# Kernel tuning notes

Hardware: AMD Instinct MI355X
Metric: run time of the kernel (lower is better)

The kernel has to match this reference:

```python
import jax, jax.numpy as jnp
import numpy as np
import math

B, S, D, H = 2, 2048, 1024, 16
DK = D // H


def setup_inputs() -> dict:
    key = jax.random.key(0)
    ks = jax.random.split(key, 12)
    scale = 1.0 / math.sqrt(D)
    inp = {
        "query": jax.random.normal(ks[0], (B, S, D), dtype=jnp.float32),
        "key": jax.random.normal(ks[1], (B, S, D), dtype=jnp.float32),
        "value": jax.random.normal(ks[2], (B, S, D), dtype=jnp.float32),
        # causal mask, broadcastable to [B, H, S, S]; 0 -> masked
        "mask": jnp.tril(jnp.ones((S, S), dtype=jnp.int32))[None, None],
        # linear params stored as [in, out] so y = x @ W + b
        "Wq": jax.random.normal(ks[3], (D, D), dtype=jnp.float32) * scale,
        "bq": jnp.zeros((D,), dtype=jnp.float32),
        "Wk": jax.random.normal(ks[4], (D, D), dtype=jnp.float32) * scale,
        "bk": jnp.zeros((D,), dtype=jnp.float32),
        "Wv": jax.random.normal(ks[5], (D, D), dtype=jnp.float32) * scale,
        "bv": jnp.zeros((D,), dtype=jnp.float32),
        "Wo": jax.random.normal(ks[6], (D, D), dtype=jnp.float32) * scale,
        "bo": jnp.zeros((D,), dtype=jnp.float32),
    }
    return inp


def reference(query, key, value, mask, Wq, bq, Wk, bk, Wv, bv, Wo, bo):
    b = query.shape[0]
    # QKV projections -> [b, H, S, DK]
    q = (query @ Wq + bq).reshape(b, -1, H, DK).transpose(0, 2, 1, 3)
    k = (key @ Wk + bk).reshape(b, -1, H, DK).transpose(0, 2, 1, 3)
    v = (value @ Wv + bv).reshape(b, -1, H, DK).transpose(0, 2, 1, 3)
    # scores [b, H, Sq, Sk]
    scores = jnp.einsum("bhqd,bhkd->bhqk", q, k) / math.sqrt(DK)
    scores = jnp.where(mask == 0, jnp.float32(-1e9), scores)
    attention_weights = jax.nn.softmax(scores, axis=-1)
    # dropout p=0.0 -> identity
    context = jnp.einsum("bhqk,bhkd->bhqd", attention_weights, v)
    context = context.transpose(0, 2, 1, 3).reshape(b, -1, H * DK)
    output = context @ Wo + bo
    return (output, attention_weights)
```

## Files before the change

### kernel.cpp

```cpp
#include <hip/hip_runtime.h>

typedef __bf16 bf16x8 __attribute__((ext_vector_type(8)));
typedef unsigned short u16x8 __attribute__((ext_vector_type(8)));
typedef unsigned short u16x4 __attribute__((ext_vector_type(4)));
typedef unsigned int u32x4 __attribute__((ext_vector_type(4)));
typedef float f32x4 __attribute__((ext_vector_type(4)));

#define MFMA16 __builtin_amdgcn_mfma_f32_16x16x32_bf16

static __device__ inline unsigned short f2bf(float f) {
    unsigned int u = __float_as_uint(f);
    u += 0x7fffu + ((u >> 16) & 1u);
    return (unsigned short)(u >> 16);
}
static __device__ inline unsigned int pack2(float a, float b) {
    return (unsigned int)f2bf(a) | ((unsigned int)f2bf(b) << 16);
}
static __device__ inline bf16x8 as_bf(u16x8 v) { return __builtin_bit_cast(bf16x8, v); }

static __device__ inline void gload_lds16(const unsigned short* g, unsigned short* l) {
    __builtin_amdgcn_global_load_lds(
        (const __attribute__((address_space(1))) void*)g,
        (__attribute__((address_space(3))) void*)l, 16, 0, 0);
}

__global__ __launch_bounds__(256) void conv3(
    const float* __restrict__ A0, const float* __restrict__ A1, const float* __restrict__ A2,
    unsigned short* __restrict__ O0, unsigned short* __restrict__ O1, unsigned short* __restrict__ O2)
{
    const float* A; unsigned short* O;
    switch (blockIdx.y) { case 0: A = A0; O = O0; break;
                          case 1: A = A1; O = O1; break;
                          default: A = A2; O = O2; break; }
    size_t i = ((size_t)blockIdx.x * 256 + threadIdx.x) * 8;
    float4 a = *(const float4*)(A + i);
    float4 b = *(const float4*)(A + i + 4);
    u16x8 o;
    o[0] = f2bf(a.x); o[1] = f2bf(a.y); o[2] = f2bf(a.z); o[3] = f2bf(a.w);
    o[4] = f2bf(b.x); o[5] = f2bf(b.y); o[6] = f2bf(b.z); o[7] = f2bf(b.w);
    *(u16x8*)(O + i) = o;
}

__global__ __launch_bounds__(256) void conv_wt(
    const float* __restrict__ W0, const float* __restrict__ W1,
    const float* __restrict__ W2, const float* __restrict__ W3,
    unsigned short* __restrict__ T0, unsigned short* __restrict__ T1,
    unsigned short* __restrict__ T2, unsigned short* __restrict__ T3)
{
    const float* W; unsigned short* T;
    switch (blockIdx.z) { case 0: W = W0; T = T0; break;
                          case 1: W = W1; T = T1; break;
                          case 2: W = W2; T = T2; break;
                          default: W = W3; T = T3; break; }
    __shared__ unsigned short L[64][72];
    int t = threadIdx.x;
    int r = t >> 2, cs = (t & 3) * 16;
    int r0 = blockIdx.y * 64, c0 = blockIdx.x * 64;
    const float* wp = W + (size_t)(r0 + r) * 1024 + c0 + cs;
    #pragma unroll
    for (int u = 0; u < 16; u += 4) {
        float4 f = *(const float4*)(wp + u);
        L[r][cs + u]     = f2bf(f.x);
        L[r][cs + u + 1] = f2bf(f.y);
        L[r][cs + u + 2] = f2bf(f.z);
        L[r][cs + u + 3] = f2bf(f.w);
    }
    __syncthreads();
    unsigned short* op = T + (size_t)(c0 + r) * 1024 + r0 + cs;
    u16x8 o0, o1;
    #pragma unroll
    for (int i2 = 0; i2 < 8; i2++) { o0[i2] = L[cs + i2][r]; o1[i2] = L[cs + 8 + i2][r]; }
    *(u16x8*)op = o0;
    *(u16x8*)(op + 8) = o1;
}

__global__ __launch_bounds__(256) void proj128(
    const unsigned short* __restrict__ Xq, const unsigned short* __restrict__ Xk,
    const unsigned short* __restrict__ Xv,
    const unsigned short* __restrict__ WqT, const unsigned short* __restrict__ WkT,
    const unsigned short* __restrict__ WvT,
    const float* __restrict__ bq, const float* __restrict__ bk, const float* __restrict__ bv,
    unsigned short* __restrict__ Qo, unsigned short* __restrict__ Ko,
    unsigned short* __restrict__ Vto)
{
    const unsigned short *X, *WT; const float* bias; float oscale;
    if (blockIdx.z == 0)      { X = Xq; WT = WqT; bias = bq; oscale = 0.125f; }
    else if (blockIdx.z == 1) { X = Xk; WT = WkT; bias = bk; oscale = 1.f; }
    else                      { X = Xv; WT = WvT; bias = bv; oscale = 1.f; }
    __shared__ __align__(16) unsigned short Al[128 * 32];
    __shared__ __align__(16) unsigned short Bl[128 * 32];
    const int tid = threadIdx.x, lane = tid & 63, wave = tid >> 6;
    const int li = lane & 15, lg = lane >> 4;
    const int wm = wave >> 1, wn = wave & 1;
    const int row0 = blockIdx.x * 128, n0 = blockIdx.y * 128;
    f32x4 acc[4][4] = {};
    const int srow = wave * 16 + (lane >> 2), sseg = lane & 3;
    const unsigned short* ga0 = X + (size_t)(row0 + srow) * 1024 + sseg * 8;
    const unsigned short* gb0 = WT + (size_t)(n0 + srow) * 1024 + sseg * 8;
    unsigned short* lA = &Al[wave * 512];
    unsigned short* lB = &Bl[wave * 512];
    for (int k0 = 0; k0 < 1024; k0 += 32) {
        gload_lds16(ga0 + k0, lA);
        gload_lds16(ga0 + 64 * 1024 + k0, lA + 2048);
        gload_lds16(gb0 + k0, lB);
        gload_lds16(gb0 + 64 * 1024 + k0, lB + 2048);
        __syncthreads();
        bf16x8 af[4], bfr[4];
        #pragma unroll
        for (int i = 0; i < 4; i++)
            af[i] = as_bf(*(const u16x8*)&Al[(wm * 64 + i * 16 + li) * 32 + lg * 8]);
        #pragma unroll
        for (int j = 0; j < 4; j++)
            bfr[j] = as_bf(*(const u16x8*)&Bl[(wn * 64 + j * 16 + li) * 32 + lg * 8]);
        #pragma unroll
        for (int i = 0; i < 4; i++)
            #pragma unroll
            for (int j = 0; j < 4; j++)
                acc[i][j] = MFMA16(af[i], bfr[j], acc[i][j], 0, 0, 0);
        __syncthreads();
    }
    const int b = row0 >> 11;
    if (blockIdx.z == 2) {
        #pragma unroll
        for (int j = 0; j < 4; j++) {
            int n = n0 + wn * 64 + j * 16 + li;
            float bb = bias[n];
            int h = n >> 6, dk = n & 63;
            unsigned short* ob = Vto + ((size_t)(b * 16 + h) * 64 + dk) * 2048;
            #pragma unroll
            for (int i = 0; i < 4; i++) {
                int s = (row0 + wm * 64 + i * 16 + lg * 4) & 2047;
                u16x4 pk;
                pk[0] = f2bf(acc[i][j][0] + bb);
                pk[1] = f2bf(acc[i][j][1] + bb);
                pk[2] = f2bf(acc[i][j][2] + bb);
                pk[3] = f2bf(acc[i][j][3] + bb);
                *(u16x4*)(ob + s) = pk;
            }
        }
    } else {
        unsigned short* out = (blockIdx.z == 0) ? Qo : Ko;
        #pragma unroll
        for (int j = 0; j < 4; j++) {
            int n = n0 + wn * 64 + j * 16 + li;
            float bb = bias[n];
            int h = n >> 6, dk = n & 63;
            unsigned short* ob = out + ((size_t)(b * 16 + h) * 2048) * 64 + dk;
            #pragma unroll
            for (int i = 0; i < 4; i++)
                #pragma unroll
                for (int r = 0; r < 4; r++) {
                    int s = (row0 + wm * 64 + i * 16 + lg * 4 + r) & 2047;
                    ob[(size_t)s * 64] = f2bf((acc[i][j][r] + bb) * oscale);
                }
        }
    }
}

__global__ __launch_bounds__(256) void final128(
    const unsigned short* __restrict__ A, const unsigned short* __restrict__ WT,
    const float* __restrict__ bias, float* __restrict__ out)
{
    __shared__ __align__(16) unsigned short Al[128 * 32];
    __shared__ __align__(16) unsigned short Bl[128 * 32];
    const int tid = threadIdx.x, lane = tid & 63, wave = tid >> 6;
    const int li = lane & 15, lg = lane >> 4;
    const int wm = wave >> 1, wn = wave & 1;
    const int row0 = blockIdx.x * 128, n0 = blockIdx.y * 128;
    f32x4 acc[4][4] = {};
    const int srow = wave * 16 + (lane >> 2), sseg = lane & 3;
    const unsigned short* ga0 = A + (size_t)(row0 + srow) * 1024 + sseg * 8;
    const unsigned short* gb0 = WT + (size_t)(n0 + srow) * 1024 + sseg * 8;
    unsigned short* lA = &Al[wave * 512];
    unsigned short* lB = &Bl[wave * 512];
    for (int k0 = 0; k0 < 1024; k0 += 32) {
        gload_lds16(ga0 + k0, lA);
        gload_lds16(ga0 + 64 * 1024 + k0, lA + 2048);
        gload_lds16(gb0 + k0, lB);
        gload_lds16(gb0 + 64 * 1024 + k0, lB + 2048);
        __syncthreads();
        bf16x8 af[4], bfr[4];
        #pragma unroll
        for (int i = 0; i < 4; i++)
            af[i] = as_bf(*(const u16x8*)&Al[(wm * 64 + i * 16 + li) * 32 + lg * 8]);
        #pragma unroll
        for (int j = 0; j < 4; j++)
            bfr[j] = as_bf(*(const u16x8*)&Bl[(wn * 64 + j * 16 + li) * 32 + lg * 8]);
        #pragma unroll
        for (int i = 0; i < 4; i++)
            #pragma unroll
            for (int j = 0; j < 4; j++)
                acc[i][j] = MFMA16(af[i], bfr[j], acc[i][j], 0, 0, 0);
        __syncthreads();
    }
    #pragma unroll
    for (int j = 0; j < 4; j++) {
        int n = n0 + wn * 64 + j * 16 + li;
        float bb = bias[n];
        #pragma unroll
        for (int i = 0; i < 4; i++)
            #pragma unroll
            for (int r = 0; r < 4; r++) {
                int row = row0 + wm * 64 + i * 16 + lg * 4 + r;
                out[(size_t)row * 1024 + n] = acc[i][j][r] + bb;
            }
    }
}

__global__ __launch_bounds__(256, 4) void attn_fused(
    const unsigned short* __restrict__ Q, const unsigned short* __restrict__ K,
    const unsigned short* __restrict__ Vt,
    float* __restrict__ wOut, unsigned short* __restrict__ ctx)
{
    __shared__ __align__(16) unsigned short Kl[2][4096];
    __shared__ __align__(16) unsigned short Vl[2][4096];
    const int tid = threadIdx.x, lane = tid & 63, wave = tid >> 6;
    const int li = lane & 15, lg = lane >> 4;
    const int y = blockIdx.y;
    const int bh = blockIdx.x * 4 + (y >> 4);
    const int t = y & 15;
    const int b = bh >> 4, h = bh & 15;
    const unsigned short* Kb = K + (size_t)bh * 2048 * 64;
    const unsigned short* Vb = Vt + (size_t)bh * 64 * 2048;
    const int aSel = 32 * (lg & 1);
    const bool hiT = lg >= 2;

    auto stageK = [&](int u, int buf) {
        const unsigned short* base = Kb + (size_t)u * 64 * 64;
        #pragma unroll
        for (int c = 0; c < 2; c++) {
            int s16 = c * 256 + wave * 64 + lane;
            int row = s16 >> 3, uu = s16 & 7;
            int ul = uu ^ (row & 7);
            gload_lds16(base + row * 64 + ul * 8,
                        &Kl[buf][(size_t)(c * 256 + wave * 64) * 8]);
        }
    };
    auto stageV = [&](int u, int buf) {
        #pragma unroll
        for (int c = 0; c < 2; c++) {
            int s16 = c * 256 + wave * 64 + lane;
            int row = s16 >> 3, uu = s16 & 7;
            int ul = uu ^ (row & 7);
            gload_lds16(Vb + (size_t)row * 2048 + u * 64 + ul * 8,
                        &Vl[buf][(size_t)(c * 256 + wave * 64) * 8]);
        }
    };
    auto kfrag = [&](const unsigned short* KB, int tt, int hf) -> bf16x8 {
        int row = tt * 16 + li;
        int st = ((hf * 4 + lg) ^ (li & 7));
        return as_bf(*(const u16x8*)&KB[row * 64 + st * 8]);
    };
    auto vfrag = [&](const unsigned short* VB, int g, int c2l) -> bf16x8 {
        int row = g * 16 + li;
        int st = ((c2l * 4 + lg) ^ (li & 7));
        return as_bf(*(const u16x8*)&VB[row * 64 + st * 8]);
    };

    #pragma unroll 1
    for (int pass = 0; pass < 2; ++pass) {
        const int Mt = pass ? (31 - t) : t;
        const int q0 = Mt * 64;
        const int M16 = Mt * 4 + wave;
        const int nun = Mt + 1;
        const unsigned short* Qp = Q + ((size_t)bh * 2048 + q0 + wave * 16 + li) * 64 + lg * 8;
        bf16x8 qa0 = as_bf(*(const u16x8*)Qp);
        bf16x8 qa1 = as_bf(*(const u16x8*)(Qp + 32));

        float lsum = 0.f;
        stageK(0, 0);
        __syncthreads();
        #pragma unroll 1
        for (int u = 0; u < nun; ++u) {
            if (u + 1 < nun) stageK(u + 1, (u + 1) & 1);
            const unsigned short* KB = &Kl[u & 1][0];
            #pragma unroll
            for (int tt = 0; tt < 4; tt++) {
                int kts = u * 4 + tt;
                if (kts <= M16) {
                    f32x4 s = {0.f, 0.f, 0.f, 0.f};
                    s = MFMA16(kfrag(KB, tt, 0), qa0, s, 0, 0, 0);
                    s = MFMA16(kfrag(KB, tt, 1), qa1, s, 0, 0, 0);
                    if (kts < M16) {
                        lsum += __expf(s[0]) + __expf(s[1]) + __expf(s[2]) + __expf(s[3]);
                    } else {
                        #pragma unroll
                        for (int r = 0; r < 4; r++)
                            if (lg * 4 + r <= li) lsum += __expf(s[r]);
                    }
                }
            }
            __syncthreads();
        }
        lsum += __shfl_xor(lsum, 16);
        lsum += __shfl_xor(lsum, 32);
        const float rinv = 1.f / lsum;

        stageK(0, 0);
        stageV(0, 0);
        __syncthreads();
        float* wRow = wOut + (size_t)bh * 2048 * 2048 + (size_t)(q0 + wave * 16 + li) * 2048;
        f32x4 o0 = {}, o1 = {}, o2 = {}, o3 = {};
        #pragma unroll 1
        for (int u = 0; u < nun; ++u) {
            if (u + 1 < nun) { stageK(u + 1, (u + 1) & 1); stageV(u + 1, (u + 1) & 1); }
            const unsigned short* KB = &Kl[u & 1][0];
            const unsigned short* VB = &Vl[u & 1][0];
            #pragma unroll
            for (int c2l = 0; c2l < 2; c2l++) {
                unsigned pk0, pk1, pk2, pk3;
                #pragma unroll
                for (int st = 0; st < 2; st++) {
                    int kts = u * 4 + c2l * 2 + st;
                    f32x4 w = {0.f, 0.f, 0.f, 0.f};
                    if (kts <= M16) {
                        f32x4 s = {0.f, 0.f, 0.f, 0.f};
                        int tt = c2l * 2 + st;
                        s = MFMA16(kfrag(KB, tt, 0), qa0, s, 0, 0, 0);
                        s = MFMA16(kfrag(KB, tt, 1), qa1, s, 0, 0, 0);
                        bool diag = (kts == M16);
                        #pragma unroll
                        for (int r = 0; r < 4; r++) {
                            float pv = __expf(s[r]);
                            if (diag && (lg * 4 + r) > li) pv = 0.f;
                            w[r] = pv * rinv;
                        }
                    }
                    *(f32x4*)(wRow + kts * 16 + lg * 4) = w;
                    if (st == 0) { pk0 = pack2(w[0], w[1]); pk1 = pack2(w[2], w[3]); }
                    else         { pk2 = pack2(w[0], w[1]); pk3 = pack2(w[2], w[3]); }
                }
                if (u * 4 + c2l * 2 <= M16) {
                    int srcA = li + aSel, srcB = srcA + 16;
                    unsigned ga0v = __shfl(pk0, srcA), ga1v = __shfl(pk1, srcA);
                    unsigned ga2v = __shfl(pk2, srcA), ga3v = __shfl(pk3, srcA);
                    unsigned gb0v = __shfl(pk0, srcB), gb1v = __shfl(pk1, srcB);
                    unsigned gb2v = __shfl(pk2, srcB), gb3v = __shfl(pk3, srcB);
                    u32x4 fr;
                    fr[0] = hiT ? ga2v : ga0v;
                    fr[1] = hiT ? ga3v : ga1v;
                    fr[2] = hiT ? gb2v : gb0v;
                    fr[3] = hiT ? gb3v : gb1v;
                    bf16x8 pa = __builtin_bit_cast(bf16x8, fr);
                    o0 = MFMA16(pa, vfrag(VB, 0, c2l), o0, 0, 0, 0);
                    o1 = MFMA16(pa, vfrag(VB, 1, c2l), o1, 0, 0, 0);
                    o2 = MFMA16(pa, vfrag(VB, 2, c2l), o2, 0, 0, 0);
                    o3 = MFMA16(pa, vfrag(VB, 3, c2l), o3, 0, 0, 0);
                }
            }
            __syncthreads();
        }
        {
            int kcov = nun * 64;
            f32x4 z = {0.f, 0.f, 0.f, 0.f};
            for (int c = kcov + lg * 4; c < 2048; c += 16)
                *(f32x4*)(wRow + c) = z;
        }
        #pragma unroll
        for (int r = 0; r < 4; r++) {
            int row = q0 + wave * 16 + lg * 4 + r;
            unsigned short* cp = ctx + (((size_t)(b * 2048 + row)) * 16 + h) * 64 + li;
            cp[0]  = f2bf(o0[r]);
            cp[16] = f2bf(o1[r]);
            cp[32] = f2bf(o2[r]);
            cp[48] = f2bf(o3[r]);
        }
    }
}

extern "C" void kernel_launch(void* const* d_in, const int* in_sizes, int n_in,
                              void* d_out, int out_size, void* d_ws, size_t ws_size,
                              hipStream_t stream) {
    const float* q_in = (const float*)d_in[0];
    const float* k_in = (const float*)d_in[1];
    const float* v_in = (const float*)d_in[2];
    const float* Wq = (const float*)d_in[4];
    const float* bq = (const float*)d_in[5];
    const float* Wk = (const float*)d_in[6];
    const float* bk = (const float*)d_in[7];
    const float* Wv = (const float*)d_in[8];
    const float* bv = (const float*)d_in[9];
    const float* Wo = (const float*)d_in[10];
    const float* bo = (const float*)d_in[11];

    float* out = (float*)d_out;
    float* wOut = out + 4194304;

    unsigned short* ws16 = (unsigned short*)d_ws;
    unsigned short* Xqb = ws16;
    unsigned short* Xkb = ws16 + 4194304;
    unsigned short* Xvb = ws16 + 8388608;
    unsigned short* WqT = ws16 + 12582912;
    unsigned short* WkT = WqT + 1048576;
    unsigned short* WvT = WkT + 1048576;
    unsigned short* WoT = WvT + 1048576;
    unsigned short* Qws = ws16 + 16777216;
    unsigned short* Kws = Qws + 4194304;
    unsigned short* Vtws = Kws + 4194304;
    unsigned short* ctxp = Vtws + 4194304;

    conv3<<<dim3(2048, 3), 256, 0, stream>>>(q_in, k_in, v_in, Xqb, Xkb, Xvb);
    conv_wt<<<dim3(16, 16, 4), 256, 0, stream>>>(Wq, Wk, Wv, Wo, WqT, WkT, WvT, WoT);
    proj128<<<dim3(32, 8, 3), 256, 0, stream>>>(Xqb, Xkb, Xvb, WqT, WkT, WvT,
                                                bq, bk, bv, Qws, Kws, Vtws);
    attn_fused<<<dim3(8, 64), 256, 0, stream>>>(Qws, Kws, Vtws, wOut, ctxp);
    final128<<<dim3(32, 8), 256, 0, stream>>>(ctxp, WoT, bo, out);
}
```

Measured before the change: 301.0 us.

## Split softmax stats into separate kernel and use 16x16x16 MFMA for PV

The row-sum pass moves out of the fused attention kernel into its own attn_stats kernel. That kernel gives each wave its own 16-row tile, balanced with a mirrored pass, and reads K straight from global memory with register prefetch instead of LDS staging and block barriers. The weight/context kernel reads the precomputed reciprocal sums. Where the 16x16x16 bf16_1k MFMA builtin exists, it feeds the probability tile directly as the A operand, removing the cross-lane shuffles needed to repack P for the 16x16x32 instruction. The cost is an extra launch, a small global buffer, and twice as many PV MFMA calls at half the K depth.

After: 352.2 us. 1.17x slower.

```diff
diff --git a/kernel.cpp b/kernel.cpp
--- a/kernel.cpp
+++ b/kernel.cpp
@@ -4,9 +4,15 @@
 typedef unsigned short u16x8 __attribute__((ext_vector_type(8)));
 typedef unsigned short u16x4 __attribute__((ext_vector_type(4)));
 typedef unsigned int u32x4 __attribute__((ext_vector_type(4)));
+typedef unsigned int u32x2 __attribute__((ext_vector_type(2)));
 typedef float f32x4 __attribute__((ext_vector_type(4)));
 
 #define MFMA16 __builtin_amdgcn_mfma_f32_16x16x32_bf16
+
+#if __has_builtin(__builtin_amdgcn_mfma_f32_16x16x16bf16_1k)
+#define HAVE_1K 1
+typedef short s16x4 __attribute__((ext_vector_type(4)));
+#endif
 
 static __device__ inline unsigned short f2bf(float f) {
     unsigned int u = __float_as_uint(f);
@@ -207,9 +213,57 @@
     }
 }
 
-__global__ __launch_bounds__(256, 4) void attn_fused(
+__global__ __launch_bounds__(256, 4) void attn_stats(
     const unsigned short* __restrict__ Q, const unsigned short* __restrict__ K,
-    const unsigned short* __restrict__ Vt,
+    float* __restrict__ rinvOut)
+{
+    const int tid = threadIdx.x, lane = tid & 63, wave = tid >> 6;
+    const int li = lane & 15, lg = lane >> 4;
+    const int y = blockIdx.y;
+    const int bh = blockIdx.x * 4 + (y >> 4);
+    const int p = (y & 15) * 4 + wave;
+    const unsigned short* Kb = K + (size_t)bh * 2048 * 64;
+
+    #pragma unroll 1
+    for (int pass = 0; pass < 2; ++pass) {
+        const int M = pass ? (127 - p) : p;
+        const int q0 = M * 16;
+        const unsigned short* Qp = Q + ((size_t)bh * 2048 + q0 + li) * 64 + lg * 8;
+        bf16x8 qa0 = as_bf(*(const u16x8*)Qp);
+        bf16x8 qa1 = as_bf(*(const u16x8*)(Qp + 32));
+        const unsigned short* kp0 = Kb + (size_t)li * 64 + lg * 8;
+
+        float lsum = 0.f;
+        u16x8 nk0 = *(const u16x8*)(kp0);
+        u16x8 nk1 = *(const u16x8*)(kp0 + 32);
+        for (int kt = 0; kt < M; ++kt) {
+            u16x8 ck0 = nk0, ck1 = nk1;
+            const unsigned short* np = kp0 + (size_t)(kt + 1) * 1024;
+            nk0 = *(const u16x8*)np;
+            nk1 = *(const u16x8*)(np + 32);
+            f32x4 s = {0.f, 0.f, 0.f, 0.f};
+            s = MFMA16(as_bf(ck0), qa0, s, 0, 0, 0);
+            s = MFMA16(as_bf(ck1), qa1, s, 0, 0, 0);
+            lsum += __expf(s[0]) + __expf(s[1]) + __expf(s[2]) + __expf(s[3]);
+        }
+        {
+            f32x4 s = {0.f, 0.f, 0.f, 0.f};
+            s = MFMA16(as_bf(nk0), qa0, s, 0, 0, 0);
+            s = MFMA16(as_bf(nk1), qa1, s, 0, 0, 0);
+            #pragma unroll
+            for (int r = 0; r < 4; r++)
+                if (lg * 4 + r <= li) lsum += __expf(s[r]);
+        }
+        lsum += __shfl_xor(lsum, 16);
+        lsum += __shfl_xor(lsum, 32);
+        if (lane < 16)
+            rinvOut[(size_t)bh * 2048 + q0 + li] = 1.f / lsum;
+    }
+}
+
+__global__ __launch_bounds__(256, 4) void attn_wctx(
+    const unsigned short* __restrict__ Q, const unsigned short* __restrict__ K,
+    const unsigned short* __restrict__ Vt, const float* __restrict__ rinvIn,
     float* __restrict__ wOut, unsigned short* __restrict__ ctx)
 {
     __shared__ __align__(16) unsigned short Kl[2][4096];
@@ -222,8 +276,10 @@
     const int b = bh >> 4, h = bh & 15;
     const unsigned short* Kb = K + (size_t)bh * 2048 * 64;
     const unsigned short* Vb = Vt + (size_t)bh * 64 * 2048;
+#ifndef HAVE_1K
     const int aSel = 32 * (lg & 1);
     const bool hiT = lg >= 2;
+#endif
 
     auto stageK = [&](int u, int buf) {
         const unsigned short* base = Kb + (size_t)u * 64 * 64;
@@ -250,11 +306,6 @@
         int row = tt * 16 + li;
         int st = ((hf * 4 + lg) ^ (li & 7));
         return as_bf(*(const u16x8*)&KB[row * 64 + st * 8]);
-    };
-    auto vfrag = [&](const unsigned short* VB, int g, int c2l) -> bf16x8 {
-        int row = g * 16 + li;
-        int st = ((c2l * 4 + lg) ^ (li & 7));
-        return as_bf(*(const u16x8*)&VB[row * 64 + st * 8]);
     };
 
     #pragma unroll 1
@@ -266,35 +317,7 @@
         const unsigned short* Qp = Q + ((size_t)bh * 2048 + q0 + wave * 16 + li) * 64 + lg * 8;
         bf16x8 qa0 = as_bf(*(const u16x8*)Qp);
         bf16x8 qa1 = as_bf(*(const u16x8*)(Qp + 32));
-
-        float lsum = 0.f;
-        stageK(0, 0);
-        __syncthreads();
-        #pragma unroll 1
-        for (int u = 0; u < nun; ++u) {
-            if (u + 1 < nun) stageK(u + 1, (u + 1) & 1);
-            const unsigned short* KB = &Kl[u & 1][0];
-            #pragma unroll
-            for (int tt = 0; tt < 4; tt++) {
-                int kts = u * 4 + tt;
-                if (kts <= M16) {
-                    f32x4 s = {0.f, 0.f, 0.f, 0.f};
-                    s = MFMA16(kfrag(KB, tt, 0), qa0, s, 0, 0, 0);
-                    s = MFMA16(kfrag(KB, tt, 1), qa1, s, 0, 0, 0);
-                    if (kts < M16) {
-                        lsum += __expf(s[0]) + __expf(s[1]) + __expf(s[2]) + __expf(s[3]);
-                    } else {
-                        #pragma unroll
-                        for (int r = 0; r < 4; r++)
-                            if (lg * 4 + r <= li) lsum += __expf(s[r]);
-                    }
-                }
-            }
-            __syncthreads();
-        }
-        lsum += __shfl_xor(lsum, 16);
-        lsum += __shfl_xor(lsum, 32);
-        const float rinv = 1.f / lsum;
+        const float rinv = rinvIn[(size_t)bh * 2048 + q0 + wave * 16 + li];
 
         stageK(0, 0);
         stageV(0, 0);
@@ -306,6 +329,40 @@
             if (u + 1 < nun) { stageK(u + 1, (u + 1) & 1); stageV(u + 1, (u + 1) & 1); }
             const unsigned short* KB = &Kl[u & 1][0];
             const unsigned short* VB = &Vl[u & 1][0];
+#ifdef HAVE_1K
+            #pragma unroll
+            for (int tt = 0; tt < 4; tt++) {
+                int kts = u * 4 + tt;
+                f32x4 w = {0.f, 0.f, 0.f, 0.f};
+                bool live = (kts <= M16);
+                if (live) {
+                    f32x4 s = {0.f, 0.f, 0.f, 0.f};
+                    s = MFMA16(kfrag(KB, tt, 0), qa0, s, 0, 0, 0);
+                    s = MFMA16(kfrag(KB, tt, 1), qa1, s, 0, 0, 0);
+                    bool diag = (kts == M16);
+                    #pragma unroll
+                    for (int r = 0; r < 4; r++) {
+                        float pv = __expf(s[r]);
+                        if (diag && (lg * 4 + r) > li) pv = 0.f;
+                        w[r] = pv * rinv;
+                    }
+                }
+                *(f32x4*)(wRow + kts * 16 + lg * 4) = w;
+                if (live) {
+                    u32x2 pq; pq[0] = pack2(w[0], w[1]); pq[1] = pack2(w[2], w[3]);
+                    s16x4 pa = __builtin_bit_cast(s16x4, pq);
+                    int slot = 2 * tt + (lg >> 1), woff = 4 * (lg & 1);
+                    #pragma unroll
+                    for (int g = 0; g < 4; g++) {
+                        int row = g * 16 + li;
+                        const unsigned short* vp = &VB[row * 64 + (slot ^ (row & 7)) * 8 + woff];
+                        s16x4 vb = __builtin_bit_cast(s16x4, *(const u16x4*)vp);
+                        f32x4* op = (g == 0) ? &o0 : (g == 1) ? &o1 : (g == 2) ? &o2 : &o3;
+                        *op = __builtin_amdgcn_mfma_f32_16x16x16bf16_1k(pa, vb, *op, 0, 0, 0);
+                    }
+                }
+            }
+#else
             #pragma unroll
             for (int c2l = 0; c2l < 2; c2l++) {
                 unsigned pk0, pk1, pk2, pk3;
@@ -342,12 +399,17 @@
                     fr[2] = hiT ? gb2v : gb0v;
                     fr[3] = hiT ? gb3v : gb1v;
                     bf16x8 pa = __builtin_bit_cast(bf16x8, fr);
-                    o0 = MFMA16(pa, vfrag(VB, 0, c2l), o0, 0, 0, 0);
-                    o1 = MFMA16(pa, vfrag(VB, 1, c2l), o1, 0, 0, 0);
-                    o2 = MFMA16(pa, vfrag(VB, 2, c2l), o2, 0, 0, 0);
-                    o3 = MFMA16(pa, vfrag(VB, 3, c2l), o3, 0, 0, 0);
+                    #pragma unroll
+                    for (int g = 0; g < 4; g++) {
+                        int row = g * 16 + li;
+                        int st2 = ((c2l * 4 + lg) ^ (li & 7));
+                        bf16x8 vb = as_bf(*(const u16x8*)&VB[row * 64 + st2 * 8]);
+                        f32x4* op = (g == 0) ? &o0 : (g == 1) ? &o1 : (g == 2) ? &o2 : &o3;
+                        *op = MFMA16(pa, vb, *op, 0, 0, 0);
+                    }
                 }
             }
+#endif
             __syncthreads();
         }
         {
@@ -398,11 +460,13 @@
     unsigned short* Kws = Qws + 4194304;
     unsigned short* Vtws = Kws + 4194304;
     unsigned short* ctxp = Vtws + 4194304;
+    float* rinvB = (float*)(ws16 + 33554432);
 
     conv3<<<dim3(2048, 3), 256, 0, stream>>>(q_in, k_in, v_in, Xqb, Xkb, Xvb);
     conv_wt<<<dim3(16, 16, 4), 256, 0, stream>>>(Wq, Wk, Wv, Wo, WqT, WkT, WvT, WoT);
     proj128<<<dim3(32, 8, 3), 256, 0, stream>>>(Xqb, Xkb, Xvb, WqT, WkT, WvT,
                                                 bq, bk, bv, Qws, Kws, Vtws);
-    attn_fused<<<dim3(8, 64), 256, 0, stream>>>(Qws, Kws, Vtws, wOut, ctxp);
+    attn_stats<<<dim3(8, 64), 256, 0, stream>>>(Qws, Kws, rinvB);
+    attn_wctx<<<dim3(8, 64), 256, 0, stream>>>(Qws, Kws, Vtws, rinvB, wOut, ctxp);
     final128<<<dim3(32, 8), 256, 0, stream>>>(ctxp, WoT, bo, out);
 }
```

## Stage attention weights in LDS for coalesced full-row global stores

Applied to the files above, without the earlier changes.

Attention probabilities are now written into a swizzled 32 KB LDS tile covering 64 rows by 128 columns. Each wave then copies contiguous 512-byte row segments to global memory, replacing the scattered 16-byte per-lane stores of the MFMA layout, and the masked-zero fill is restructured so each wave writes whole rows. The goal is better write coalescing on the 2048x2048 fp32 weights output, which likely dominates traffic. The cost is extra LDS traffic and barriers, and launch bounds drop from 4 to 2 blocks per SM, so occupancy falls.

Measured after the change: 267.5 us. 11.1% less time.

```diff
diff --git a/kernel.cpp b/kernel.cpp
--- a/kernel.cpp
+++ b/kernel.cpp
@@ -207,13 +207,14 @@
     }
 }
 
-__global__ __launch_bounds__(256, 4) void attn_fused(
+__global__ __launch_bounds__(256, 2) void attn_fused(
     const unsigned short* __restrict__ Q, const unsigned short* __restrict__ K,
     const unsigned short* __restrict__ Vt,
     float* __restrict__ wOut, unsigned short* __restrict__ ctx)
 {
     __shared__ __align__(16) unsigned short Kl[2][4096];
     __shared__ __align__(16) unsigned short Vl[2][4096];
+    __shared__ __align__(16) float Pst[64 * 128];
     const int tid = threadIdx.x, lane = tid & 63, wave = tid >> 6;
     const int li = lane & 15, lg = lane >> 4;
     const int y = blockIdx.y;
@@ -222,6 +223,7 @@
     const int b = bh >> 4, h = bh & 15;
     const unsigned short* Kb = K + (size_t)bh * 2048 * 64;
     const unsigned short* Vb = Vt + (size_t)bh * 64 * 2048;
+    float* wHead = wOut + (size_t)bh * 2048 * 2048;
     const int aSel = 32 * (lg & 1);
     const bool hiT = lg >= 2;
 
@@ -263,6 +265,7 @@
         const int q0 = Mt * 64;
         const int M16 = Mt * 4 + wave;
         const int nun = Mt + 1;
+        const int nun2 = (nun + 1) & ~1;
         const unsigned short* Qp = Q + ((size_t)bh * 2048 + q0 + wave * 16 + li) * 64 + lg * 8;
         bf16x8 qa0 = as_bf(*(const u16x8*)Qp);
         bf16x8 qa1 = as_bf(*(const u16x8*)(Qp + 32));
@@ -299,62 +302,85 @@
         stageK(0, 0);
         stageV(0, 0);
         __syncthreads();
-        float* wRow = wOut + (size_t)bh * 2048 * 2048 + (size_t)(q0 + wave * 16 + li) * 2048;
         f32x4 o0 = {}, o1 = {}, o2 = {}, o3 = {};
+        const int prow = wave * 16 + li;
         #pragma unroll 1
-        for (int u = 0; u < nun; ++u) {
-            if (u + 1 < nun) { stageK(u + 1, (u + 1) & 1); stageV(u + 1, (u + 1) & 1); }
-            const unsigned short* KB = &Kl[u & 1][0];
-            const unsigned short* VB = &Vl[u & 1][0];
-            #pragma unroll
-            for (int c2l = 0; c2l < 2; c2l++) {
-                unsigned pk0, pk1, pk2, pk3;
+        for (int v = 0; v < (nun2 >> 1); ++v) {
+            #pragma unroll
+            for (int half = 0; half < 2; ++half) {
+                const int u = 2 * v + half;
+                if (u + 1 < nun) { stageK(u + 1, (u + 1) & 1); stageV(u + 1, (u + 1) & 1); }
+                const unsigned short* KB = &Kl[u & 1][0];
+                const unsigned short* VB = &Vl[u & 1][0];
                 #pragma unroll
-                for (int st = 0; st < 2; st++) {
-                    int kts = u * 4 + c2l * 2 + st;
-                    f32x4 w = {0.f, 0.f, 0.f, 0.f};
-                    if (kts <= M16) {
-                        f32x4 s = {0.f, 0.f, 0.f, 0.f};
-                        int tt = c2l * 2 + st;
-                        s = MFMA16(kfrag(KB, tt, 0), qa0, s, 0, 0, 0);
-                        s = MFMA16(kfrag(KB, tt, 1), qa1, s, 0, 0, 0);
-                        bool diag = (kts == M16);
-                        #pragma unroll
-                        for (int r = 0; r < 4; r++) {
-                            float pv = __expf(s[r]);
-                            if (diag && (lg * 4 + r) > li) pv = 0.f;
-                            w[r] = pv * rinv;
+                for (int c2l = 0; c2l < 2; c2l++) {
+                    unsigned pk0, pk1, pk2, pk3;
+                    #pragma unroll
+                    for (int st = 0; st < 2; st++) {
+                        int kts = u * 4 + c2l * 2 + st;
+                        f32x4 w = {0.f, 0.f, 0.f, 0.f};
+                        if (kts <= M16) {
+                            f32x4 s = {0.f, 0.f, 0.f, 0.f};
+                            int tt = c2l * 2 + st;
+                            s = MFMA16(kfrag(KB, tt, 0), qa0, s, 0, 0, 0);
+                            s = MFMA16(kfrag(KB, tt, 1), qa1, s, 0, 0, 0);
+                            bool diag = (kts == M16);
+                            #pragma unroll
+                            for (int r = 0; r < 4; r++) {
+                                float pv = __expf(s[r]);
+                                if (diag && (lg * 4 + r) > li) pv = 0.f;
+                                w[r] = pv * rinv;
+                            }
                         }
+                        int slot = half * 16 + (c2l * 2 + st) * 4 + lg;
+                        *(f32x4*)&Pst[prow * 128 + (slot ^ (li & 7)) * 4] = w;
+                        if (st == 0) { pk0 = pack2(w[0], w[1]); pk1 = pack2(w[2], w[3]); }
+                        else         { pk2 = pack2(w[0], w[1]); pk3 = pack2(w[2], w[3]); }
                     }
-                    *(f32x4*)(wRow + kts * 16 + lg * 4) = w;
-                    if (st == 0) { pk0 = pack2(w[0], w[1]); pk1 = pack2(w[2], w[3]); }
-                    else         { pk2 = pack2(w[0], w[1]); pk3 = pack2(w[2], w[3]); }
+                    if (u * 4 + c2l * 2 <= M16) {
+                        int srcA = li + aSel, srcB = srcA + 16;
+                        unsigned ga0v = __shfl(pk0, srcA), ga1v = __shfl(pk1, srcA);
+                        unsigned ga2v = __shfl(pk2, srcA), ga3v = __shfl(pk3, srcA);
+                        unsigned gb0v = __shfl(pk0, srcB), gb1v = __shfl(pk1, srcB);
+                        unsigned gb2v = __shfl(pk2, srcB), gb3v = __shfl(pk3, srcB);
+                        u32x4 fr;
+                        fr[0] = hiT ? ga2v : ga0v;
+                        fr[1] = hiT ? ga3v : ga1v;
+                        fr[2] = hiT ? gb2v : gb0v;
+                        fr[3] = hiT ? gb3v : gb1v;
+                        bf16x8 pa = __builtin_bit_cast(bf16x8, fr);
+                        o0 = MFMA16(pa, vfrag(VB, 0, c2l), o0, 0, 0, 0);
+                        o1 = MFMA16(pa, vfrag(VB, 1, c2l), o1, 0, 0, 0);
+                        o2 = MFMA16(pa, vfrag(VB, 2, c2l), o2, 0, 0, 0);
+                        o3 = MFMA16(pa, vfrag(VB, 3, c2l), o3, 0, 0, 0);
+                    }
                 }
-                if (u * 4 + c2l * 2 <= M16) {
-                    int srcA = li + aSel, srcB = srcA + 16;
-                    unsigned ga0v = __shfl(pk0, srcA), ga1v = __shfl(pk1, srcA);
-                    unsigned ga2v = __shfl(pk2, srcA), ga3v = __shfl(pk3, srcA);
-                    unsigned gb0v = __shfl(pk0, srcB), gb1v = __shfl(pk1, srcB);
-                    unsigned gb2v = __shfl(pk2, srcB), gb3v = __shfl(pk3, srcB);
-                    u32x4 fr;
-                    fr[0] = hiT ? ga2v : ga0v;
-                    fr[1] = hiT ? ga3v : ga1v;
-                    fr[2] = hiT ? gb2v : gb0v;
-                    fr[3] = hiT ? gb3v : gb1v;
-                    bf16x8 pa = __builtin_bit_cast(bf16x8, fr);
-                    o0 = MFMA16(pa, vfrag(VB, 0, c2l), o0, 0, 0, 0);
-                    o1 = MFMA16(pa, vfrag(VB, 1, c2l), o1, 0, 0, 0);
-                    o2 = MFMA16(pa, vfrag(VB, 2, c2l), o2, 0, 0, 0);
-                    o3 = MFMA16(pa, vfrag(VB, 3, c2l), o3, 0, 0, 0);
+                __syncthreads();
+            }
+            {
+                const int colb = v * 128;
+                const int slot = lane & 31;
+                const int rsub = lane >> 5;
+                #pragma unroll
+                for (int i = 0; i < 8; ++i) {
+                    int row = wave * 2 + i * 8 + rsub;
+                    f32x4 val = *(const f32x4*)&Pst[row * 128 + ((slot ^ (row & 7)) * 4)];
+                    *(f32x4*)(wHead + (size_t)(q0 + row) * 2048 + colb + slot * 4) = val;
                 }
             }
             __syncthreads();
         }
         {
-            int kcov = nun * 64;
+            const int kcov2 = nun2 * 64;
             f32x4 z = {0.f, 0.f, 0.f, 0.f};
-            for (int c = kcov + lg * 4; c < 2048; c += 16)
-                *(f32x4*)(wRow + c) = z;
+            #pragma unroll 1
+            for (int rr = 0; rr < 16; ++rr) {
+                float* bp = wHead + (size_t)(q0 + wave * 16 + rr) * 2048;
+                for (int cb = kcov2; cb < 2048; cb += 256) {
+                    int c = cb + lane * 4;
+                    if (c < 2048) *(f32x4*)(bp + c) = z;
+                }
+            }
         }
         #pragma unroll
         for (int r = 0; r < 4; r++) {
```

## Stage attention weights through LDS for coalesced stores, one tile per block

Applied to the files above, without the earlier changes.

Each block now handles a single 64-row query tile instead of a balanced pair of tiles. Blocks are ordered longest-first across a grid twice as large. The normalized probabilities are written to a swizzled LDS buffer and then stored row-contiguously to the weights output, replacing scattered 16-byte strided global stores. V is read straight from global memory instead of being staged through LDS. The intent is to cut the cost of the large weights write, which dominates traffic, at the price of extra barriers per step and uncached direct V loads. The masked-region zero fill is also reorganised to be lane-contiguous per row.

Result: no change. 304.2 us (+1.1%).

```diff
diff --git a/kernel.cpp b/kernel.cpp
--- a/kernel.cpp
+++ b/kernel.cpp
@@ -213,15 +213,19 @@
     float* __restrict__ wOut, unsigned short* __restrict__ ctx)
 {
     __shared__ __align__(16) unsigned short Kl[2][4096];
-    __shared__ __align__(16) unsigned short Vl[2][4096];
+    __shared__ __align__(16) float Pst[64 * 64];
     const int tid = threadIdx.x, lane = tid & 63, wave = tid >> 6;
     const int li = lane & 15, lg = lane >> 4;
     const int y = blockIdx.y;
-    const int bh = blockIdx.x * 4 + (y >> 4);
-    const int t = y & 15;
+    const int bh = blockIdx.x * 4 + (y & 3);
+    const int T = 31 - (y >> 2);
     const int b = bh >> 4, h = bh & 15;
+    const int q0 = T * 64;
+    const int M16 = T * 4 + wave;
+    const int nun = T + 1;
     const unsigned short* Kb = K + (size_t)bh * 2048 * 64;
     const unsigned short* Vb = Vt + (size_t)bh * 64 * 2048;
+    float* wHead = wOut + (size_t)bh * 2048 * 2048;
     const int aSel = 32 * (lg & 1);
     const bool hiT = lg >= 2;
 
@@ -236,135 +240,126 @@
                         &Kl[buf][(size_t)(c * 256 + wave * 64) * 8]);
         }
     };
-    auto stageV = [&](int u, int buf) {
-        #pragma unroll
-        for (int c = 0; c < 2; c++) {
-            int s16 = c * 256 + wave * 64 + lane;
-            int row = s16 >> 3, uu = s16 & 7;
-            int ul = uu ^ (row & 7);
-            gload_lds16(Vb + (size_t)row * 2048 + u * 64 + ul * 8,
-                        &Vl[buf][(size_t)(c * 256 + wave * 64) * 8]);
-        }
-    };
     auto kfrag = [&](const unsigned short* KB, int tt, int hf) -> bf16x8 {
         int row = tt * 16 + li;
         int st = ((hf * 4 + lg) ^ (li & 7));
         return as_bf(*(const u16x8*)&KB[row * 64 + st * 8]);
     };
-    auto vfrag = [&](const unsigned short* VB, int g, int c2l) -> bf16x8 {
-        int row = g * 16 + li;
-        int st = ((c2l * 4 + lg) ^ (li & 7));
-        return as_bf(*(const u16x8*)&VB[row * 64 + st * 8]);
-    };
-
+
+    const unsigned short* Qp = Q + ((size_t)bh * 2048 + q0 + wave * 16 + li) * 64 + lg * 8;
+    bf16x8 qa0 = as_bf(*(const u16x8*)Qp);
+    bf16x8 qa1 = as_bf(*(const u16x8*)(Qp + 32));
+
+    float lsum = 0.f;
+    stageK(0, 0);
+    __syncthreads();
     #pragma unroll 1
-    for (int pass = 0; pass < 2; ++pass) {
-        const int Mt = pass ? (31 - t) : t;
-        const int q0 = Mt * 64;
-        const int M16 = Mt * 4 + wave;
-        const int nun = Mt + 1;
-        const unsigned short* Qp = Q + ((size_t)bh * 2048 + q0 + wave * 16 + li) * 64 + lg * 8;
-        bf16x8 qa0 = as_bf(*(const u16x8*)Qp);
-        bf16x8 qa1 = as_bf(*(const u16x8*)(Qp + 32));
-
-        float lsum = 0.f;
-        stageK(0, 0);
-        __syncthreads();
-        #pragma unroll 1
-        for (int u = 0; u < nun; ++u) {
-            if (u + 1 < nun) stageK(u + 1, (u + 1) & 1);
-            const unsigned short* KB = &Kl[u & 1][0];
-            #pragma unroll
-            for (int tt = 0; tt < 4; tt++) {
+    for (int u = 0; u < nun; ++u) {
+        if (u + 1 < nun) stageK(u + 1, (u + 1) & 1);
+        const unsigned short* KB = &Kl[u & 1][0];
+        #pragma unroll
+        for (int tt = 0; tt < 4; tt++) {
+            int kts = u * 4 + tt;
+            if (kts <= M16) {
+                f32x4 s = {0.f, 0.f, 0.f, 0.f};
+                s = MFMA16(kfrag(KB, tt, 0), qa0, s, 0, 0, 0);
+                s = MFMA16(kfrag(KB, tt, 1), qa1, s, 0, 0, 0);
+                if (kts < M16) {
+                    lsum += __expf(s[0]) + __expf(s[1]) + __expf(s[2]) + __expf(s[3]);
+                } else {
+                    #pragma unroll
+                    for (int r = 0; r < 4; r++)
+                        if (lg * 4 + r <= li) lsum += __expf(s[r]);
+                }
+            }
+        }
+        __syncthreads();
+    }
+    lsum += __shfl_xor(lsum, 16);
+    lsum += __shfl_xor(lsum, 32);
+    const float rinv = 1.f / lsum;
+
+    stageK(0, 0);
+    __syncthreads();
+    f32x4 o0 = {}, o1 = {}, o2 = {}, o3 = {};
+    const int prow = wave * 16 + li;
+    #pragma unroll 1
+    for (int u = 0; u < nun; ++u) {
+        if (u + 1 < nun) stageK(u + 1, (u + 1) & 1);
+        const unsigned short* KB = &Kl[u & 1][0];
+        #pragma unroll
+        for (int c2l = 0; c2l < 2; c2l++) {
+            unsigned pk0, pk1, pk2, pk3;
+            #pragma unroll
+            for (int st = 0; st < 2; st++) {
+                int tt = c2l * 2 + st;
                 int kts = u * 4 + tt;
+                f32x4 w = {0.f, 0.f, 0.f, 0.f};
                 if (kts <= M16) {
                     f32x4 s = {0.f, 0.f, 0.f, 0.f};
                     s = MFMA16(kfrag(KB, tt, 0), qa0, s, 0, 0, 0);
                     s = MFMA16(kfrag(KB, tt, 1), qa1, s, 0, 0, 0);
-                    if (kts < M16) {
-                        lsum += __expf(s[0]) + __expf(s[1]) + __expf(s[2]) + __expf(s[3]);
-                    } else {
-                        #pragma unroll
-                        for (int r = 0; r < 4; r++)
-                            if (lg * 4 + r <= li) lsum += __expf(s[r]);
+                    bool diag = (kts == M16);
+                    #pragma unroll
+                    for (int r = 0; r < 4; r++) {
+                        float pv = __expf(s[r]);
+                        if (diag && (lg * 4 + r) > li) pv = 0.f;
+                        w[r] = pv * rinv;
                     }
                 }
-            }
-            __syncthreads();
-        }
-        lsum += __shfl_xor(lsum, 16);
-        lsum += __shfl_xor(lsum, 32);
-        const float rinv = 1.f / lsum;
-
-        stageK(0, 0);
-        stageV(0, 0);
-        __syncthreads();
-        float* wRow = wOut + (size_t)bh * 2048 * 2048 + (size_t)(q0 + wave * 16 + li) * 2048;
-        f32x4 o0 = {}, o1 = {}, o2 = {}, o3 = {};
+                *(f32x4*)&Pst[prow * 64 + ((tt * 4 + lg) ^ (li & 7)) * 4] = w;
+                if (st == 0) { pk0 = pack2(w[0], w[1]); pk1 = pack2(w[2], w[3]); }
+                else         { pk2 = pack2(w[0], w[1]); pk3 = pack2(w[2], w[3]); }
+            }
+            if (u * 4 + c2l * 2 <= M16) {
+                int srcA = li + aSel, srcB = srcA + 16;
+                unsigned ga0v = __shfl(pk0, srcA), ga1v = __shfl(pk1, srcA);
+                unsigned ga2v = __shfl(pk2, srcA), ga3v = __shfl(pk3, srcA);
+                unsigned gb0v = __shfl(pk0, srcB), gb1v = __shfl(pk1, srcB);
+                unsigned gb2v = __shfl(pk2, srcB), gb3v = __shfl(pk3, srcB);
+                u32x4 fr;
+                fr[0] = hiT ? ga2v : ga0v;
+                fr[1] = hiT ? ga3v : ga1v;
+                fr[2] = hiT ? gb2v : gb0v;
+                fr[3] = hiT ? gb3v : gb1v;
+                bf16x8 pa = __builtin_bit_cast(bf16x8, fr);
+                const unsigned short* vp = Vb + (size_t)li * 2048 + u * 64 + c2l * 32 + lg * 8;
+                o0 = MFMA16(pa, as_bf(*(const u16x8*)(vp)),             o0, 0, 0, 0);
+                o1 = MFMA16(pa, as_bf(*(const u16x8*)(vp + 16 * 2048)), o1, 0, 0, 0);
+                o2 = MFMA16(pa, as_bf(*(const u16x8*)(vp + 32 * 2048)), o2, 0, 0, 0);
+                o3 = MFMA16(pa, as_bf(*(const u16x8*)(vp + 48 * 2048)), o3, 0, 0, 0);
+            }
+        }
+        __syncthreads();
+        #pragma unroll
+        for (int i = 0; i < 4; ++i) {
+            int idx = i * 256 + tid;
+            int row = idx >> 4, slot = idx & 15;
+            f32x4 val = *(const f32x4*)&Pst[row * 64 + ((slot ^ (row & 7)) * 4)];
+            *(f32x4*)(wHead + (size_t)(q0 + row) * 2048 + u * 64 + slot * 4) = val;
+        }
+        __syncthreads();
+    }
+    {
+        const int kcov = nun * 64;
+        f32x4 z = {0.f, 0.f, 0.f, 0.f};
         #pragma unroll 1
-        for (int u = 0; u < nun; ++u) {
-            if (u + 1 < nun) { stageK(u + 1, (u + 1) & 1); stageV(u + 1, (u + 1) & 1); }
-            const unsigned short* KB = &Kl[u & 1][0];
-            const unsigned short* VB = &Vl[u & 1][0];
-            #pragma unroll
-            for (int c2l = 0; c2l < 2; c2l++) {
-                unsigned pk0, pk1, pk2, pk3;
-                #pragma unroll
-                for (int st = 0; st < 2; st++) {
-                    int kts = u * 4 + c2l * 2 + st;
-                    f32x4 w = {0.f, 0.f, 0.f, 0.f};
-                    if (kts <= M16) {
-                        f32x4 s = {0.f, 0.f, 0.f, 0.f};
-                        int tt = c2l * 2 + st;
-                        s = MFMA16(kfrag(KB, tt, 0), qa0, s, 0, 0, 0);
-                        s = MFMA16(kfrag(KB, tt, 1), qa1, s, 0, 0, 0);
-                        bool diag = (kts == M16);
-                        #pragma unroll
-                        for (int r = 0; r < 4; r++) {
-                            float pv = __expf(s[r]);
-                            if (diag && (lg * 4 + r) > li) pv = 0.f;
-                            w[r] = pv * rinv;
-                        }
-                    }
-                    *(f32x4*)(wRow + kts * 16 + lg * 4) = w;
-                    if (st == 0) { pk0 = pack2(w[0], w[1]); pk1 = pack2(w[2], w[3]); }
-                    else         { pk2 = pack2(w[0], w[1]); pk3 = pack2(w[2], w[3]); }
-                }
-                if (u * 4 + c2l * 2 <= M16) {
-                    int srcA = li + aSel, srcB = srcA + 16;
-                    unsigned ga0v = __shfl(pk0, srcA), ga1v = __shfl(pk1, srcA);
-                    unsigned ga2v = __shfl(pk2, srcA), ga3v = __shfl(pk3, srcA);
-                    unsigned gb0v = __shfl(pk0, srcB), gb1v = __shfl(pk1, srcB);
-                    unsigned gb2v = __shfl(pk2, srcB), gb3v = __shfl(pk3, srcB);
-                    u32x4 fr;
-                    fr[0] = hiT ? ga2v : ga0v;
-                    fr[1] = hiT ? ga3v : ga1v;
-                    fr[2] = hiT ? gb2v : gb0v;
-                    fr[3] = hiT ? gb3v : gb1v;
-                    bf16x8 pa = __builtin_bit_cast(bf16x8, fr);
-                    o0 = MFMA16(pa, vfrag(VB, 0, c2l), o0, 0, 0, 0);
-                    o1 = MFMA16(pa, vfrag(VB, 1, c2l), o1, 0, 0, 0);
-                    o2 = MFMA16(pa, vfrag(VB, 2, c2l), o2, 0, 0, 0);
-                    o3 = MFMA16(pa, vfrag(VB, 3, c2l), o3, 0, 0, 0);
-                }
-            }
-            __syncthreads();
-        }
-        {
-            int kcov = nun * 64;
-            f32x4 z = {0.f, 0.f, 0.f, 0.f};
-            for (int c = kcov + lg * 4; c < 2048; c += 16)
-                *(f32x4*)(wRow + c) = z;
-        }
-        #pragma unroll
-        for (int r = 0; r < 4; r++) {
-            int row = q0 + wave * 16 + lg * 4 + r;
-            unsigned short* cp = ctx + (((size_t)(b * 2048 + row)) * 16 + h) * 64 + li;
-            cp[0]  = f2bf(o0[r]);
-            cp[16] = f2bf(o1[r]);
-            cp[32] = f2bf(o2[r]);
-            cp[48] = f2bf(o3[r]);
-        }
+        for (int rr = 0; rr < 16; ++rr) {
+            float* bp = wHead + (size_t)(q0 + wave * 16 + rr) * 2048;
+            for (int cb = kcov; cb < 2048; cb += 256) {
+                int c = cb + lane * 4;
+                if (c < 2048) *(f32x4*)(bp + c) = z;
+            }
+        }
+    }
+    #pragma unroll
+    for (int r = 0; r < 4; r++) {
+        int row = q0 + wave * 16 + lg * 4 + r;
+        unsigned short* cp = ctx + (((size_t)(b * 2048 + row)) * 16 + h) * 64 + li;
+        cp[0]  = f2bf(o0[r]);
+        cp[16] = f2bf(o1[r]);
+        cp[32] = f2bf(o2[r]);
+        cp[48] = f2bf(o3[r]);
     }
 }
 
@@ -403,6 +398,6 @@
     conv_wt<<<dim3(16, 16, 4), 256, 0, stream>>>(Wq, Wk, Wv, Wo, WqT, WkT, WvT, WoT);
     proj128<<<dim3(32, 8, 3), 256, 0, stream>>>(Xqb, Xkb, Xvb, WqT, WkT, WvT,
                                                 bq, bk, bv, Qws, Kws, Vtws);
-    attn_fused<<<dim3(8, 64), 256, 0, stream>>>(Qws, Kws, Vtws, wOut, ctxp);
+    attn_fused<<<dim3(8, 128), 256, 0, stream>>>(Qws, Kws, Vtws, wOut, ctxp);
     final128<<<dim3(32, 8), 256, 0, stream>>>(ctxp, WoT, bo, out);
 }
```
